# Performance work log

Measured on AMD Instinct MI355X. Metric: run time of the kernel, lower is better.

The kernel has to match this reference:

```python
import jax, jax.numpy as jnp
import numpy as np

H, NH, NKV, D, I, T, B = 4096, 32, 8, 128, 12288, 1024, 128
THETA, EPS = 1e6, 1e-6


def setup_inputs() -> dict:
    ks = iter(jax.random.split(jax.random.key(0), 64))

    def randn(s):
        return jax.random.normal(next(ks), s, jnp.float32)

    def qw(o, i):
        return jax.random.randint(next(ks), (o, i), 0, 16, jnp.int32)

    def sc(o, g):
        return jax.random.uniform(next(ks), (o, g), jnp.float32, 0.005, 0.02)

    def rot(g):  # block-diagonal rotation, one 128x128 block per input group
        return randn((g, B, B)) / np.float32(np.sqrt(B))

    return dict(
        positions=jnp.arange(T, dtype=jnp.int32),
        hidden_states=randn((T, H)),
        residual=randn((T, H)),
        w_in=jnp.ones(H, jnp.float32), w_post=jnp.ones(H, jnp.float32),
        w_qn=jnp.ones(D, jnp.float32), w_kn=jnp.ones(D, jnp.float32),
        R_q=rot(H // B), qw_q=qw(NH * D, H), sc_q=sc(NH * D, H // B),
        R_k=rot(H // B), qw_k=qw(NKV * D, H), sc_k=sc(NKV * D, H // B),
        R_v=rot(H // B), qw_v=qw(NKV * D, H), sc_v=sc(NKV * D, H // B),
        R_o=rot(NH * D // B), qw_o=qw(H, NH * D), sc_o=sc(H, NH * D // B),
        R_g=rot(H // B), qw_g=qw(I, H), sc_g=sc(I, H // B),
        R_u=rot(H // B), qw_u=qw(I, H), sc_u=sc(I, H // B),
        R_d=rot(I // B), qw_d=qw(H, I), sc_d=sc(H, I // B),
    )


def _rmsnorm(x, w):
    return x * jax.lax.rsqrt(jnp.mean(x * x, -1, keepdims=True) + EPS) * w


def _rot_lin(x, R, qw, sc):
    # RotateLinearInt4: block-rotate input, then int4 group-dequant GEMM.
    G = R.shape[0]
    xr = jnp.einsum('tgi,gij->tgj', x.reshape(-1, G, B), R).reshape(x.shape)
    O = qw.shape[0]
    W = ((qw.astype(x.dtype) - 8.0).reshape(O, G, B) * sc[:, :, None]).reshape(O, G * B)
    return xr @ W.T


def _rope(pos, x):  # neox-style rope, x: [T, h, D]
    half = D // 2
    inv = jnp.power(jnp.float32(THETA), -(jnp.arange(half, dtype=jnp.float32) * (2.0 / D)))
    f = pos.astype(jnp.float32)[:, None] * inv  # [T, half]
    cos, sin = jnp.cos(f)[:, None, :], jnp.sin(f)[:, None, :]
    x1, x2 = x[..., :half], x[..., half:]
    return jnp.concatenate([x1 * cos - x2 * sin, x2 * cos + x1 * sin], -1)


def _forward(positions, hidden_states, residual, w_in, w_post, w_qn, w_kn,
             R_q, qw_q, sc_q, R_k, qw_k, sc_k, R_v, qw_v, sc_v,
             R_o, qw_o, sc_o, R_g, qw_g, sc_g, R_u, qw_u, sc_u,
             R_d, qw_d, sc_d):
    res = hidden_states + residual            # fused add+RMSNorm path
    x = _rmsnorm(res, w_in)
    q = _rot_lin(x, R_q, qw_q, sc_q).reshape(T, NH, D)
    k = _rot_lin(x, R_k, qw_k, sc_k).reshape(T, NKV, D)
    v = _rot_lin(x, R_v, qw_v, sc_v).reshape(T, NKV, D)
    q = _rmsnorm(q, w_qn)                     # per-head q/k RMSNorm
    k = _rmsnorm(k, w_kn)
    q = _rope(positions, q)
    k = _rope(positions, k)
    rep = NH // NKV                           # GQA: repeat kv heads
    kk = jnp.repeat(k, rep, axis=1)
    vv = jnp.repeat(v, rep, axis=1)
    scores = jnp.einsum('thd,shd->hts', q, kk) * (D ** -0.5)
    mask = jnp.tril(jnp.ones((T, T), bool))
    scores = jnp.where(mask, scores, jnp.finfo(scores.dtype).min)
    probs = jax.nn.softmax(scores, -1)
    attn = jnp.einsum('hts,shd->thd', probs, vv).reshape(T, NH * D)
    h = _rot_lin(attn, R_o, qw_o, sc_o)
    res2 = h + res
    x2 = _rmsnorm(res2, w_post)
    gate = _rot_lin(x2, R_g, qw_g, sc_g)
    up = _rot_lin(x2, R_u, qw_u, sc_u)
    h2 = _rot_lin(jax.nn.silu(gate) * up, R_d, qw_d, sc_d)
    return h2, res2


def reference(positions, hidden_states, residual, w_in, w_post, w_qn, w_kn,
              R_q, qw_q, sc_q, R_k, qw_k, sc_k, R_v, qw_v, sc_v,
              R_o, qw_o, sc_o, R_g, qw_g, sc_g, R_u, qw_u, sc_u,
              R_d, qw_d, sc_d):
    return _forward(positions, hidden_states, residual, w_in, w_post, w_qn, w_kn,
                    R_q, qw_q, sc_q, R_k, qw_k, sc_k, R_v, qw_v, sc_v,
                    R_o, qw_o, sc_o, R_g, qw_g, sc_g, R_u, qw_u, sc_u,
                    R_d, qw_d, sc_d)
```

## Files before the change

kernel.cpp:

```cpp
#include <hip/hip_runtime.h>

typedef unsigned short u16;
typedef __attribute__((ext_vector_type(4))) float   f32x4;
typedef __attribute__((ext_vector_type(8))) __bf16  bf16x8;
typedef __attribute__((ext_vector_type(4))) __bf16  bf16x4;
typedef __attribute__((ext_vector_type(8))) short   short8;
typedef __attribute__((ext_vector_type(4))) int     int32x4;
typedef __attribute__((ext_vector_type(4))) short   short4v;

#define MFMA16(a,b,c) __builtin_amdgcn_mfma_f32_16x16x32_bf16(a,b,c,0,0,0)

static __device__ __forceinline__ u16 f2bf(float f){
  unsigned u = __builtin_bit_cast(unsigned, f);
  return (u16)((u + 0x7fffu + ((u >> 16) & 1u)) >> 16);
}
static __device__ __forceinline__ float bf2f(u16 h){
  return __builtin_bit_cast(float, ((unsigned)h) << 16);
}
static __device__ __forceinline__ bf16x8 ldb16(const u16* p){
  return __builtin_bit_cast(bf16x8, *(const short8*)p);
}
static __device__ __forceinline__ void gload_lds16(const void* g, void* l){
  __builtin_amdgcn_global_load_lds(
      reinterpret_cast<const __attribute__((address_space(1))) unsigned int*>(
          reinterpret_cast<unsigned long long>(g)),
      reinterpret_cast<__attribute__((address_space(3))) unsigned int*>(
          reinterpret_cast<unsigned long long>(l)),
      16, 0, 0);
}

static constexpr int T_ = 1024, H_ = 4096, NH_ = 32, NKV_ = 8, I_ = 12288;

__global__ __launch_bounds__(256) void addnorm_kernel(
    const float* __restrict__ a, const float* __restrict__ b,
    const float* __restrict__ w, float* __restrict__ res_out,
    u16* __restrict__ x_out)
{
  const int t = blockIdx.x, tid = threadIdx.x;
  __shared__ float red[4];
  float vals[16]; float ss = 0.f;
  const size_t base = (size_t)t * H_;
  #pragma unroll
  for (int i = 0; i < 16; ++i){
    int c = tid + i*256;
    float v = a[base + c];
    if (b) v += b[base + c];
    vals[i] = v; ss += v*v;
  }
  #pragma unroll
  for (int off = 32; off; off >>= 1) ss += __shfl_xor(ss, off);
  if ((tid & 63) == 0) red[tid >> 6] = ss;
  __syncthreads();
  float tot = red[0] + red[1] + red[2] + red[3];
  float rn = rsqrtf(tot / (float)H_ + 1e-6f);
  #pragma unroll
  for (int i = 0; i < 16; ++i){
    int c = tid + i*256;
    if (res_out) res_out[base + c] = vals[i];
    x_out[base + c] = f2bf(vals[i] * rn * w[c]);
  }
}

__global__ __launch_bounds__(256) void rprep_kernel(
    const float* __restrict__ Rq, const float* __restrict__ Rk,
    const float* __restrict__ Rv, const float* __restrict__ Ro,
    const float* __restrict__ Rg_, const float* __restrict__ Ru,
    const float* __restrict__ Rd, u16* __restrict__ Rt)
{
  __shared__ float sR[128][129];
  const int b = blockIdx.x, tid = threadIdx.x;
  const float* src;
  if      (b <  32) src = Rq  + (size_t)(b      ) * 16384;
  else if (b <  64) src = Rk  + (size_t)(b -  32) * 16384;
  else if (b <  96) src = Rv  + (size_t)(b -  64) * 16384;
  else if (b < 128) src = Ro  + (size_t)(b -  96) * 16384;
  else if (b < 160) src = Rg_ + (size_t)(b - 128) * 16384;
  else if (b < 192) src = Ru  + (size_t)(b - 160) * 16384;
  else              src = Rd  + (size_t)(b - 192) * 16384;
  #pragma unroll
  for (int it = 0; it < 16; ++it){
    int idx = (it*256 + tid) * 4;
    float4 v = *(const float4*)&src[idx];
    int i = idx >> 7, j = idx & 127;
    sR[i][j] = v.x; sR[i][j+1] = v.y; sR[i][j+2] = v.z; sR[i][j+3] = v.w;
  }
  __syncthreads();
  u16* dst = Rt + (size_t)b * 16384;
  #pragma unroll
  for (int it = 0; it < 32; ++it){
    int idx = it*256 + tid;
    int j = idx >> 6, i2 = (idx & 63) * 2;
    unsigned lo = f2bf(sR[i2][j]), hi = f2bf(sR[i2+1][j]);
    *(unsigned*)&dst[j*128 + i2] = lo | (hi << 16);
  }
}

__global__ __launch_bounds__(256) void rot_kernel(
    const u16* __restrict__ X, const u16* __restrict__ Rt,
    u16* __restrict__ Y0, u16* __restrict__ Y1, u16* __restrict__ Y2,
    int LD, int gpt, const u16* __restrict__ X2)
{
  __shared__ u16 sX[64][136];
  __shared__ u16 sRt[128][136];
  const int by = blockIdx.y, g = by % gpt;
  const int m0 = blockIdx.x * 64, tid = threadIdx.x;
  u16* Y = (by < gpt) ? Y0 : (by < 2*gpt ? Y1 : Y2);
  #pragma unroll
  for (int i = 0; i < 4; ++i){
    int vid = i*256 + tid, r = vid >> 4, c = (vid & 15) * 8;
    size_t gaddr = (size_t)(m0 + r) * LD + g*128 + c;
    short8 vx = *(const short8*)&X[gaddr];
    if (X2){
      short8 vu = *(const short8*)&X2[gaddr];
      const u16* px = (const u16*)&vx;
      const u16* pu = (const u16*)&vu;
      short8 o;
      u16* po = (u16*)&o;
      #pragma unroll
      for (int e = 0; e < 8; ++e){
        float gv = bf2f(px[e]), uv = bf2f(pu[e]);
        po[e] = f2bf(gv / (1.f + __expf(-gv)) * uv);
      }
      *(short8*)&sX[r][c] = o;
    } else {
      *(short8*)&sX[r][c] = vx;
    }
  }
  const u16* Rg = Rt + (size_t)by * 16384;
  #pragma unroll
  for (int it = 0; it < 8; ++it){
    int idx = it*256 + tid;
    int j = idx >> 4, c8 = (idx & 15) * 8;
    *(short8*)&sRt[j][c8] = *(const short8*)&Rg[j*128 + c8];
  }
  __syncthreads();
  const int lane = tid & 63, w = tid >> 6;
  const int fr = lane & 15, fq = lane >> 4, nw = w * 32;
  f32x4 acc[4][2];
  #pragma unroll
  for (int mi=0;mi<4;mi++)
    #pragma unroll
    for (int ni=0;ni<2;ni++) acc[mi][ni] = (f32x4){0.f,0.f,0.f,0.f};
  #pragma unroll
  for (int kk = 0; kk < 128; kk += 32){
    bf16x8 af[4], bv[2];
    #pragma unroll
    for (int mi=0;mi<4;mi++) af[mi] = ldb16(&sX[mi*16 + fr][kk + fq*8]);
    #pragma unroll
    for (int ni=0;ni<2;ni++) bv[ni] = ldb16(&sRt[nw + ni*16 + fr][kk + fq*8]);
    #pragma unroll
    for (int mi=0;mi<4;mi++)
      #pragma unroll
      for (int ni=0;ni<2;ni++)
        acc[mi][ni] = MFMA16(af[mi], bv[ni], acc[mi][ni]);
  }
  #pragma unroll
  for (int mi=0;mi<4;mi++)
    #pragma unroll
    for (int ni=0;ni<2;ni++)
      #pragma unroll
      for (int rg=0;rg<4;rg++){
        int m = m0 + mi*16 + fq*4 + rg;
        int n = g*128 + nw + ni*16 + fr;
        Y[(size_t)m * LD + n] = f2bf(acc[mi][ni][rg]);
      }
}

template<int NF, bool PARTIAL, bool OUT_BF16>
__global__ __launch_bounds__(512, 1) void gemm_deq(
    const u16* __restrict__ A, const int* __restrict__ QW,
    const float* __restrict__ SC, void* __restrict__ Cout,
    int N, int K, int kc, int nN)
{
  __shared__ u16 sA[2][16384];
  __shared__ u16 sB[2][NF * 4096];
  const int tid = threadIdx.x;
  const int lane = tid & 63, w = tid >> 6;
  const int nblk = gridDim.x, q8 = nblk >> 3, b = blockIdx.x;
  const int l = (b & 7) * q8 + (b >> 3);
  const int mt = l & 3, rest = l >> 2;
  const int nt = rest % nN, z = rest / nN;
  const int bm0 = mt * 256, bn0 = nt * (NF * 64);
  const int kbase = z * kc;
  const int KG = K >> 7;
  const int nkt = kc >> 6;

  f32x4 acc[8][NF];
  #pragma unroll
  for (int i=0;i<8;i++)
    #pragma unroll
    for (int j=0;j<NF;j++) acc[i][j] = (f32x4){0.f,0.f,0.f,0.f};

  const int wr = (w >> 2) * 128, wc = (w & 3) * (NF * 16);
  const int fr = lane & 15, fq = lane >> 4;

  const int l8 = lane >> 3;
  const size_t K2 = (size_t)K * 2;
  const char* gA0 = (const char*)A
      + ((size_t)(bm0 + w*32 + l8) * K + (size_t)kbase) * 2
      + (((lane & 7) * 16) ^ (l8 << 4));
  auto ADMA = [&](int kt, int c){
    const char* g = gA0 + (size_t)kt * 128;
    char* lb = (char*)&sA[c][0] + (w*32) * 128;
    #pragma unroll
    for (int i=0;i<4;i++)
      gload_lds16(g + (size_t)(i*8) * K2, lb + i*1024);
  };

  const int rBr = tid >> 4, cB4 = (tid & 15) * 4;
  const int* gB0 = QW + (size_t)(bn0 + rBr) * K + kbase + cB4;
  const float* gS0 = SC + (size_t)(bn0 + rBr) * KG;
  const int sBx = (cB4 * 2) ^ ((rBr & 7) << 4);

  int32x4 rB[2*NF];
  float   rS[2*NF];
  auto loadB = [&](int kt){
    const int* gb = gB0 + kt*64;
    const int g = (kbase + kt*64) >> 7;
    const float* ps = gS0 + g;
    #pragma unroll
    for (int i=0;i<2*NF;i++){
      rB[i] = *(const int32x4*)(gb + (size_t)i*32*K);
      rS[i] = ps[(size_t)i*32*KG];
    }
  };
  auto storeB = [&](int c){
    #pragma unroll
    for (int i=0;i<2*NF;i++){
      float s = rS[i], ns = -8.f * s;
      bf16x4 o;
      o[0] = (__bf16)fmaf((float)rB[i].x, s, ns);
      o[1] = (__bf16)fmaf((float)rB[i].y, s, ns);
      o[2] = (__bf16)fmaf((float)rB[i].z, s, ns);
      o[3] = (__bf16)fmaf((float)rB[i].w, s, ns);
      *(bf16x4*)((char*)&sB[c][0] + (rBr + 32*i)*128 + sBx) = o;
    }
  };

  auto mfma_half = [&](int c, int kk){
    bf16x8 af[8], bv[NF];
    #pragma unroll
    for (int mi=0;mi<8;mi++){
      int r = wr + mi*16 + fr;
      af[mi] = *(const bf16x8*)((const char*)&sA[c][0] + r*128 +
                ((kk*64 + fq*16) ^ ((r & 7) << 4)));
    }
    #pragma unroll
    for (int ni=0;ni<NF;ni++){
      int r = wc + ni*16 + fr;
      bv[ni] = *(const bf16x8*)((const char*)&sB[c][0] + r*128 +
                ((kk*64 + fq*16) ^ ((r & 7) << 4)));
    }
    __builtin_amdgcn_s_setprio(1);
    #pragma unroll
    for (int mi=0;mi<8;mi++)
      #pragma unroll
      for (int ni=0;ni<NF;ni++)
        acc[mi][ni] = MFMA16(af[mi], bv[ni], acc[mi][ni]);
    __builtin_amdgcn_s_setprio(0);
  };

  loadB(0);
  ADMA(0, 0);
  asm volatile("s_waitcnt vmcnt(4)" ::: "memory");
  __builtin_amdgcn_sched_barrier(0);
  storeB(0);
  asm volatile("s_waitcnt vmcnt(0) lgkmcnt(0)" ::: "memory");
  __builtin_amdgcn_s_barrier();

  int cb = 0;
  for (int t = 0; t < nkt; ++t){
    const bool more = (t + 1) < nkt;
    if (more){
      loadB(t+1);
      ADMA(t+1, cb ^ 1);
      __builtin_amdgcn_sched_barrier(0);
    }
    mfma_half(cb, 0);
    mfma_half(cb, 1);
    if (more){
      asm volatile("s_waitcnt vmcnt(4)" ::: "memory");
      __builtin_amdgcn_sched_barrier(0);
      storeB(cb ^ 1);
      asm volatile("s_waitcnt vmcnt(0) lgkmcnt(0)" ::: "memory");
      __builtin_amdgcn_sched_barrier(0);
      __builtin_amdgcn_s_barrier();
      cb ^= 1;
    }
  }

  #pragma unroll
  for (int mi=0;mi<8;mi++)
    #pragma unroll
    for (int ni=0;ni<NF;ni++)
      #pragma unroll
      for (int rg=0;rg<4;rg++){
        size_t m = bm0 + wr + mi*16 + fq*4 + rg;
        size_t n = bn0 + wc + ni*16 + fr;
        float v = acc[mi][ni][rg];
        if (PARTIAL)          ((float*)Cout)[((size_t)z*1024 + m) * N + n] = v;
        else if (OUT_BF16)    ((u16*)Cout)[m * N + n] = f2bf(v);
        else                  ((float*)Cout)[m * N + n] = v;
      }
}

__global__ __launch_bounds__(256) void reduce_splits(
    const float* __restrict__ P, int nsplit, int n,
    const float* __restrict__ addend, float* __restrict__ outf, u16* __restrict__ outb)
{
  size_t base = ((size_t)blockIdx.x*256 + threadIdx.x) * 4;
  if (base >= (size_t)n) return;
  f32x4 s = *(const f32x4*)&P[base];
  for (int j = 1; j < nsplit; ++j)
    s += *(const f32x4*)&P[(size_t)j*n + base];
  if (addend) s += *(const f32x4*)&addend[base];
  if (outb){
    short4v o;
    #pragma unroll
    for (int e=0;e<4;e++) o[e] = (short)f2bf(s[e]);
    *(short4v*)&outb[base] = o;
  } else {
    *(f32x4*)&outf[base] = s;
  }
}

__global__ __launch_bounds__(64) void qknorm_rope_kernel(
    const float* __restrict__ in, const float* __restrict__ w,
    const int* __restrict__ pos, u16* __restrict__ out, int nh)
{
  const int t = blockIdx.x, h = blockIdx.y, j = threadIdx.x;
  const float* row = in + ((size_t)t * nh + h) * 128;
  float x1 = row[j], x2 = row[j + 64];
  float ss = x1*x1 + x2*x2;
  #pragma unroll
  for (int off = 32; off; off >>= 1) ss += __shfl_xor(ss, off);
  float rn = rsqrtf(ss / 128.f + 1e-6f);
  float xn1 = x1 * rn * w[j], xn2 = x2 * rn * w[j + 64];
  float inv = exp2f(-(float)j * (19.93156856932417f / 64.f));
  float f = (float)pos[t] * inv;
  float sv, cv; sincosf(f, &sv, &cv);
  u16* orow = out + ((size_t)t * nh + h) * 128;
  orow[j]      = f2bf(xn1 * cv - xn2 * sv);
  orow[j + 64] = f2bf(xn2 * cv + xn1 * sv);
}

__global__ __launch_bounds__(256) void attn_kernel(
    const u16* __restrict__ Q, const u16* __restrict__ Kc,
    const u16* __restrict__ Vc, u16* __restrict__ O)
{
  __shared__ u16 sK[32][136];
  __shared__ u16 sVt[128][40];
  __shared__ u16 sP[4][16][40];
  const int b = blockIdx.x;
  const int qt = (b < 256) ? (b & 15) : (15 - (b & 15));
  const int h = b >> 4;
  const int kvh = h >> 2;
  const int tid = threadIdx.x, lane = tid & 63, w = tid >> 6;
  const int fr = lane & 15, fq = lane >> 4;
  const int r0 = qt*64 + w*16;
  const float scale = 0.08838834764831845f;
  bf16x8 aq[4];
  #pragma unroll
  for (int kd=0;kd<4;kd++)
    aq[kd] = ldb16(&Q[(size_t)(r0 + fr) * 4096 + h*128 + kd*32 + fq*8]);
  f32x4 accO[8];
  #pragma unroll
  for (int ni=0;ni<8;ni++) accO[ni] = (f32x4){0.f,0.f,0.f,0.f};
  float mrow[4] = {-1e30f,-1e30f,-1e30f,-1e30f};
  float lrow[4] = {0.f,0.f,0.f,0.f};
  const int ntiles = (qt + 1) * 2;
  for (int jt = 0; jt < ntiles; ++jt){
    __syncthreads();
    #pragma unroll
    for (int i=0;i<2;i++){
      int vid = i*256 + tid, r = vid >> 4, c = (vid & 15) * 8;
      *(short8*)&sK[r][c] = *(const short8*)&Kc[(size_t)(jt*32 + r) * 1024 + kvh*128 + c];
      short8 vv = *(const short8*)&Vc[(size_t)(jt*32 + r) * 1024 + kvh*128 + c];
      const u16* pv = (const u16*)&vv;
      #pragma unroll
      for (int e=0;e<8;e++) sVt[c + e][r] = pv[e];
    }
    __syncthreads();
    f32x4 accS[2]; accS[0] = (f32x4){0.f,0.f,0.f,0.f}; accS[1] = accS[0];
    #pragma unroll
    for (int kd=0;kd<4;kd++){
      #pragma unroll
      for (int ni=0;ni<2;ni++){
        bf16x8 bk = ldb16(&sK[ni*16 + fr][kd*32 + fq*8]);
        accS[ni] = MFMA16(aq[kd], bk, accS[ni]);
      }
    }
    float s[2][4];
    #pragma unroll
    for (int ni=0;ni<2;ni++)
      #pragma unroll
      for (int rg=0;rg<4;rg++){
        int row = r0 + fq*4 + rg, col = jt*32 + ni*16 + fr;
        float v = accS[ni][rg] * scale;
        s[ni][rg] = (col <= row) ? v : -1e30f;
      }
    float alpha[4];
    #pragma unroll
    for (int rg=0;rg<4;rg++){
      float mx = fmaxf(s[0][rg], s[1][rg]);
      #pragma unroll
      for (int off=1; off<16; off<<=1) mx = fmaxf(mx, __shfl_xor(mx, off, 16));
      float mnew = fmaxf(mrow[rg], mx);
      alpha[rg] = __expf(mrow[rg] - mnew);
      mrow[rg] = mnew;
      float p0 = __expf(s[0][rg] - mnew), p1 = __expf(s[1][rg] - mnew);
      s[0][rg] = p0; s[1][rg] = p1;
      float ps = p0 + p1;
      #pragma unroll
      for (int off=1; off<16; off<<=1) ps += __shfl_xor(ps, off, 16);
      lrow[rg] = lrow[rg] * alpha[rg] + ps;
    }
    #pragma unroll
    for (int ni=0;ni<2;ni++)
      #pragma unroll
      for (int rg=0;rg<4;rg++)
        sP[w][fq*4 + rg][ni*16 + fr] = f2bf(s[ni][rg]);
    __syncthreads();
    #pragma unroll
    for (int ni=0;ni<8;ni++)
      #pragma unroll
      for (int rg=0;rg<4;rg++) accO[ni][rg] *= alpha[rg];
    bf16x8 ap = ldb16(&sP[w][fr][fq*8]);
    #pragma unroll
    for (int ni=0;ni<8;ni++){
      bf16x8 bv = ldb16(&sVt[ni*16 + fr][fq*8]);
      accO[ni] = MFMA16(ap, bv, accO[ni]);
    }
  }
  #pragma unroll
  for (int ni=0;ni<8;ni++)
    #pragma unroll
    for (int rg=0;rg<4;rg++){
      int row = r0 + fq*4 + rg, col = h*128 + ni*16 + fr;
      O[(size_t)row * 4096 + col] = f2bf(accO[ni][rg] / lrow[rg]);
    }
}

extern "C" void kernel_launch(void* const* d_in, const int* in_sizes, int n_in,
                              void* d_out, int out_size, void* d_ws, size_t ws_size,
                              hipStream_t stream)
{
  const int*   positions = (const int*)  d_in[0];
  const float* hs    = (const float*)d_in[1];
  const float* resid = (const float*)d_in[2];
  const float* w_in  = (const float*)d_in[3];
  const float* w_post= (const float*)d_in[4];
  const float* w_qn  = (const float*)d_in[5];
  const float* w_kn  = (const float*)d_in[6];
  const float* R_q = (const float*)d_in[7];
  const int*   qw_q= (const int*)  d_in[8];
  const float* sc_q= (const float*)d_in[9];
  const float* R_k = (const float*)d_in[10];
  const int*   qw_k= (const int*)  d_in[11];
  const float* sc_k= (const float*)d_in[12];
  const float* R_v = (const float*)d_in[13];
  const int*   qw_v= (const int*)  d_in[14];
  const float* sc_v= (const float*)d_in[15];
  const float* R_o = (const float*)d_in[16];
  const int*   qw_o= (const int*)  d_in[17];
  const float* sc_o= (const float*)d_in[18];
  const float* R_g = (const float*)d_in[19];
  const int*   qw_g= (const int*)  d_in[20];
  const float* sc_g= (const float*)d_in[21];
  const float* R_u = (const float*)d_in[22];
  const int*   qw_u= (const int*)  d_in[23];
  const float* sc_u= (const float*)d_in[24];
  const float* R_d = (const float*)d_in[25];
  const int*   qw_d= (const int*)  d_in[26];
  const float* sc_d= (const float*)d_in[27];
  (void)in_sizes; (void)n_in; (void)out_size; (void)ws_size;

  char* wsp = (char*)d_ws; size_t off = 0;
  auto alloc = [&](size_t bytes)->void*{
    void* p = wsp + off; off += (bytes + 255) & ~(size_t)255; return p;
  };
  float* res  = (float*)alloc((size_t)T_*H_*4);
  u16*   xbf  = (u16*)  alloc((size_t)T_*H_*2);
  u16*   xrA  = (u16*)  alloc((size_t)T_*H_*2);
  u16*   xrB  = (u16*)  alloc((size_t)T_*H_*2);
  u16*   xrC  = (u16*)  alloc((size_t)T_*H_*2);
  float* qf   = (float*)alloc((size_t)T_*4096*4);
  float* kf   = (float*)alloc((size_t)T_*1024*4);
  u16*   qbf  = (u16*)  alloc((size_t)T_*4096*2);
  u16*   kbf  = (u16*)  alloc((size_t)T_*1024*2);
  u16*   vbf  = (u16*)  alloc((size_t)T_*1024*2);
  u16*   abf  = (u16*)  alloc((size_t)T_*4096*2);
  u16*   gbf  = (u16*)  alloc((size_t)T_*I_*2);
  u16*   ubf  = (u16*)  alloc((size_t)T_*I_*2);
  u16*   hbf  = (u16*)  alloc((size_t)T_*I_*2);
  u16*   Rtb  = (u16*)  alloc((size_t)288*16384*2);

  float* pQKV = (float*)gbf;
  float* pO   = (float*)gbf;
  float* pD   = (float*)wsp;

  float* h2   = (float*)d_out;
  float* res2 = (float*)d_out + (size_t)T_*H_;

  rprep_kernel<<<288, 256, 0, stream>>>(R_q, R_k, R_v, R_o, R_g, R_u, R_d, Rtb);
  addnorm_kernel<<<T_, 256, 0, stream>>>(hs, resid, w_in, res, xbf);
  rot_kernel<<<dim3(16,96),256,0,stream>>>(xbf, Rtb, xrA, xrB, xrC, H_, 32, nullptr);
  gemm_deq<4,true ,false><<<256,512,0,stream>>>(xrA, qw_q, sc_q, pQKV, 4096, 4096, 1024, 16);
  reduce_splits<<<(T_*4096)/1024,256,0,stream>>>(pQKV, 4, T_*4096, nullptr, qf, nullptr);
  gemm_deq<4,true ,false><<<256,512,0,stream>>>(xrB, qw_k, sc_k, pQKV, 1024, 4096, 256, 4);
  reduce_splits<<<(T_*1024)/1024,256,0,stream>>>(pQKV, 16, T_*1024, nullptr, kf, nullptr);
  gemm_deq<4,true ,false><<<256,512,0,stream>>>(xrC, qw_v, sc_v, pQKV, 1024, 4096, 256, 4);
  reduce_splits<<<(T_*1024)/1024,256,0,stream>>>(pQKV, 16, T_*1024, nullptr, nullptr, vbf);
  qknorm_rope_kernel<<<dim3(T_,NH_ ),64,0,stream>>>(qf, w_qn, positions, qbf, NH_);
  qknorm_rope_kernel<<<dim3(T_,NKV_),64,0,stream>>>(kf, w_kn, positions, kbf, NKV_);
  attn_kernel<<<512,256,0,stream>>>(qbf, kbf, vbf, abf);
  rot_kernel<<<dim3(16,32),256,0,stream>>>(abf, Rtb + (size_t)96*16384, xrA, nullptr, nullptr, H_, 32, nullptr);
  gemm_deq<4,true ,false><<<256,512,0,stream>>>(xrA, qw_o, sc_o, pO, 4096, 4096, 1024, 16);
  reduce_splits<<<(T_*4096)/1024,256,0,stream>>>(pO, 4, T_*4096, res, res2, nullptr);
  addnorm_kernel<<<T_,256,0,stream>>>(res2, nullptr, w_post, nullptr, xbf);
  rot_kernel<<<dim3(16,64),256,0,stream>>>(xbf, Rtb + (size_t)128*16384, xrA, xrB, nullptr, H_, 32, nullptr);
  gemm_deq<3,false,true ><<<256,512,0,stream>>>(xrA, qw_g, sc_g, gbf, 12288, 4096, 4096, 64);
  gemm_deq<3,false,true ><<<256,512,0,stream>>>(xrB, qw_u, sc_u, ubf, 12288, 4096, 4096, 64);
  rot_kernel<<<dim3(16,96),256,0,stream>>>(gbf, Rtb + (size_t)192*16384, hbf, nullptr, nullptr, I_, 96, ubf);
  gemm_deq<4,true ,false><<<256,512,0,stream>>>(hbf, qw_d, sc_d, pD, 4096, 12288, 3072, 16);
  reduce_splits<<<(T_*4096)/1024,256,0,stream>>>(pD, 4, T_*4096, nullptr, h2, nullptr);
}
```

Before: 834.7 us.

## Fuse split-K reductions into qk-norm/rope and post-attn addnorm; deepen B prefetch

The standalone reduce_splits passes for Q, K and the O projection are removed. qknorm_rope and a new addnorm_red kernel now sum the partial results directly, which cuts launches and intermediate fp32 round trips. The dequant GEMM mainloop now issues the quantized-weight loads two k-tiles ahead. It waits on them with partial vmcnt counts instead of draining all outstanding loads each iteration, to overlap memory with MFMA. The hard-coded vmcnt values depend on the exact count of loads issued, so a miscount could cause races.

```diff
diff --git a/kernel.cpp b/kernel.cpp
--- a/kernel.cpp
+++ b/kernel.cpp
@@ -57,6 +57,37 @@
   for (int i = 0; i < 16; ++i){
     int c = tid + i*256;
     if (res_out) res_out[base + c] = vals[i];
+    x_out[base + c] = f2bf(vals[i] * rn * w[c]);
+  }
+}
+
+__global__ __launch_bounds__(256) void addnorm_red_kernel(
+    const float* __restrict__ P, int nsplit,
+    const float* __restrict__ resd, const float* __restrict__ w,
+    float* __restrict__ res_out, u16* __restrict__ x_out)
+{
+  const int t = blockIdx.x, tid = threadIdx.x;
+  __shared__ float red[4];
+  float vals[16]; float ss = 0.f;
+  const size_t base = (size_t)t * H_;
+  const size_t stride = (size_t)T_ * H_;
+  #pragma unroll
+  for (int i = 0; i < 16; ++i){
+    int c = tid + i*256;
+    float v = resd[base + c];
+    for (int z = 0; z < nsplit; ++z) v += P[(size_t)z*stride + base + c];
+    vals[i] = v; ss += v*v;
+  }
+  #pragma unroll
+  for (int off = 32; off; off >>= 1) ss += __shfl_xor(ss, off);
+  if ((tid & 63) == 0) red[tid >> 6] = ss;
+  __syncthreads();
+  float tot = red[0] + red[1] + red[2] + red[3];
+  float rn = rsqrtf(tot / (float)H_ + 1e-6f);
+  #pragma unroll
+  for (int i = 0; i < 16; ++i){
+    int c = tid + i*256;
+    res_out[base + c] = vals[i];
     x_out[base + c] = f2bf(vals[i] * rn * w[c]);
   }
 }
@@ -260,34 +291,50 @@
     __builtin_amdgcn_s_setprio(0);
   };
 
+#define WAIT_ADMA() do { if (NF==3) asm volatile("s_waitcnt vmcnt(12)" ::: "memory"); \
+                         else       asm volatile("s_waitcnt vmcnt(16)" ::: "memory"); } while(0)
+
   loadB(0);
   ADMA(0, 0);
   asm volatile("s_waitcnt vmcnt(4)" ::: "memory");
   __builtin_amdgcn_sched_barrier(0);
   storeB(0);
-  asm volatile("s_waitcnt vmcnt(0) lgkmcnt(0)" ::: "memory");
+  if (nkt > 1){ loadB(1); __builtin_amdgcn_sched_barrier(0); }
+  WAIT_ADMA();
+  asm volatile("s_waitcnt lgkmcnt(0)" ::: "memory");
   __builtin_amdgcn_s_barrier();
 
   int cb = 0;
   for (int t = 0; t < nkt; ++t){
-    const bool more = (t + 1) < nkt;
+    const bool more  = (t + 1) < nkt;
+    const bool more2 = (t + 2) < nkt;
     if (more){
-      loadB(t+1);
       ADMA(t+1, cb ^ 1);
       __builtin_amdgcn_sched_barrier(0);
     }
     mfma_half(cb, 0);
-    mfma_half(cb, 1);
     if (more){
       asm volatile("s_waitcnt vmcnt(4)" ::: "memory");
       __builtin_amdgcn_sched_barrier(0);
       storeB(cb ^ 1);
-      asm volatile("s_waitcnt vmcnt(0) lgkmcnt(0)" ::: "memory");
+      __builtin_amdgcn_sched_barrier(0);
+    }
+    mfma_half(cb, 1);
+    if (more){
+      if (more2){
+        loadB(t+2);
+        __builtin_amdgcn_sched_barrier(0);
+        WAIT_ADMA();
+      } else {
+        asm volatile("s_waitcnt vmcnt(0)" ::: "memory");
+      }
+      asm volatile("s_waitcnt lgkmcnt(0)" ::: "memory");
       __builtin_amdgcn_sched_barrier(0);
       __builtin_amdgcn_s_barrier();
       cb ^= 1;
     }
   }
+#undef WAIT_ADMA
 
   #pragma unroll
   for (int mi=0;mi<8;mi++)
@@ -324,13 +371,19 @@
   }
 }
 
-__global__ __launch_bounds__(64) void qknorm_rope_kernel(
-    const float* __restrict__ in, const float* __restrict__ w,
-    const int* __restrict__ pos, u16* __restrict__ out, int nh)
+__global__ __launch_bounds__(64) void qknorm_rope_red(
+    const float* __restrict__ P, int nsplit, int nh,
+    const float* __restrict__ w, const int* __restrict__ pos, u16* __restrict__ out)
 {
   const int t = blockIdx.x, h = blockIdx.y, j = threadIdx.x;
-  const float* row = in + ((size_t)t * nh + h) * 128;
-  float x1 = row[j], x2 = row[j + 64];
+  const int N = nh * 128;
+  const size_t stride = (size_t)T_ * N;
+  const size_t base = (size_t)t * N + h*128;
+  float x1 = 0.f, x2 = 0.f;
+  for (int z = 0; z < nsplit; ++z){
+    x1 += P[(size_t)z*stride + base + j];
+    x2 += P[(size_t)z*stride + base + j + 64];
+  }
   float ss = x1*x1 + x2*x2;
   #pragma unroll
   for (int off = 32; off; off >>= 1) ss += __shfl_xor(ss, off);
@@ -494,6 +547,7 @@
   u16*   ubf  = (u16*)  alloc((size_t)T_*I_*2);
   u16*   hbf  = (u16*)  alloc((size_t)T_*I_*2);
   u16*   Rtb  = (u16*)  alloc((size_t)288*16384*2);
+  (void)qf; (void)kf;
 
   float* pQKV = (float*)gbf;
   float* pO   = (float*)gbf;
@@ -506,18 +560,15 @@
   addnorm_kernel<<<T_, 256, 0, stream>>>(hs, resid, w_in, res, xbf);
   rot_kernel<<<dim3(16,96),256,0,stream>>>(xbf, Rtb, xrA, xrB, xrC, H_, 32, nullptr);
   gemm_deq<4,true ,false><<<256,512,0,stream>>>(xrA, qw_q, sc_q, pQKV, 4096, 4096, 1024, 16);
-  reduce_splits<<<(T_*4096)/1024,256,0,stream>>>(pQKV, 4, T_*4096, nullptr, qf, nullptr);
+  qknorm_rope_red<<<dim3(T_,NH_ ),64,0,stream>>>(pQKV, 4, NH_, w_qn, positions, qbf);
   gemm_deq<4,true ,false><<<256,512,0,stream>>>(xrB, qw_k, sc_k, pQKV, 1024, 4096, 256, 4);
-  reduce_splits<<<(T_*1024)/1024,256,0,stream>>>(pQKV, 16, T_*1024, nullptr, kf, nullptr);
+  qknorm_rope_red<<<dim3(T_,NKV_),64,0,stream>>>(pQKV, 16, NKV_, w_kn, positions, kbf);
   gemm_deq<4,true ,false><<<256,512,0,stream>>>(xrC, qw_v, sc_v, pQKV, 1024, 4096, 256, 4);
   reduce_splits<<<(T_*1024)/1024,256,0,stream>>>(pQKV, 16, T_*1024, nullptr, nullptr, vbf);
-  qknorm_rope_kernel<<<dim3(T_,NH_ ),64,0,stream>>>(qf, w_qn, positions, qbf, NH_);
-  qknorm_rope_kernel<<<dim3(T_,NKV_),64,0,stream>>>(kf, w_kn, positions, kbf, NKV_);
   attn_kernel<<<512,256,0,stream>>>(qbf, kbf, vbf, abf);
   rot_kernel<<<dim3(16,32),256,0,stream>>>(abf, Rtb + (size_t)96*16384, xrA, nullptr, nullptr, H_, 32, nullptr);
   gemm_deq<4,true ,false><<<256,512,0,stream>>>(xrA, qw_o, sc_o, pO, 4096, 4096, 1024, 16);
-  reduce_splits<<<(T_*4096)/1024,256,0,stream>>>(pO, 4, T_*4096, res, res2, nullptr);
-  addnorm_kernel<<<T_,256,0,stream>>>(res2, nullptr, w_post, nullptr, xbf);
+  addnorm_red_kernel<<<T_,256,0,stream>>>(pO, 4, res, w_post, res2, xbf);
   rot_kernel<<<dim3(16,64),256,0,stream>>>(xbf, Rtb + (size_t)128*16384, xrA, xrB, nullptr, H_, 32, nullptr);
   gemm_deq<3,false,true ><<<256,512,0,stream>>>(xrA, qw_g, sc_g, gbf, 12288, 4096, 4096, 64);
   gemm_deq<3,false,true ><<<256,512,0,stream>>>(xrB, qw_u, sc_u, ubf, 12288, 4096, 4096, 64);
```

New measurement: 809.2 us, median of 3. 3.1% less time.
